# Kernel tuning notes

Hardware: AMD Instinct MI355X
Metric: run time of the kernel (lower is better)

Reference implementation:

```python
import jax, jax.numpy as jnp
import numpy as np

EPS = 0.01    # halting threshold eps
MU = 2.0      # halting probability multiplier
N_MAX = 16    # static upper bound on ACT steps (loop halts in 1-2 steps w/ bias=1, mu=2)

# Binarize: hard threshold at 1-eps forward, straight-through (identity) backward
@jax.custom_vjp
def binarize(x):
    return (x >= 1.0 - EPS).astype(x.dtype)

def _bin_fwd(x):
    return binarize(x), None

def _bin_bwd(_, g):
    return (g,)

binarize.defvjp(_bin_fwd, _bin_bwd)


def setup_inputs() -> dict:
    key = jax.random.key(0)
    ks = jax.random.split(key, 12)
    I, H, O = 4095, 4096, 4096
    sc = 1.0 / np.sqrt(H)
    u = lambda k, s: jax.random.uniform(k, s, jnp.float32, -sc, sc)
    return {
        "x": jax.random.normal(ks[0], (I,), jnp.float32),
        "s0": jax.random.normal(ks[1], (H,), jnp.float32) * 0.1,
        "y0": jax.random.normal(ks[2], (O,), jnp.float32),
        "h0": jnp.zeros((1,), jnp.float32),
        # nn.RNN (tanh) single layer params
        "W_ih": u(ks[3], (H, 1 + I)),
        "b_ih": u(ks[4], (H,)),
        "W_hh": u(ks[5], (H, H)),
        "b_hh": u(ks[6], (H,)),
        # fc_halt (bias hard-set to 1.0 in __init__)
        "W_halt": u(ks[7], (1, H)),
        "b_halt": jnp.ones((1,), jnp.float32),
        # fc_output
        "W_out": u(ks[8], (O, H)),
        "b_out": u(ks[9], (O,)),
    }


def reference(x, s0, y0, h0, W_ih, b_ih, W_hh, b_hh, W_halt, b_halt, W_out, b_out):
    x0 = jnp.concatenate([jnp.zeros((1,), x.dtype), x])  # skip-flag 0 input
    x1 = jnp.concatenate([jnp.ones((1,), x.dtype), x])   # skip-flag 1 input (first step)

    def step(carry, t):
        s, acc = carry
        xin = jnp.where(t == 0, x1, x0)
        valid = acc[0] < 1.0 - EPS  # ACT while-loop condition at step start
        s_new = jnp.tanh(W_ih @ xin + b_ih + W_hh @ s + b_hh)  # tanh RNN cell
        y_new = W_out @ s_new + b_out
        acc_new = acc + MU * jax.nn.sigmoid(W_halt @ s_new + b_halt)
        s_next = jnp.where(valid, s_new, s)
        acc_next = jnp.where(valid, acc_new, acc)
        return (s_next, acc_next), (s_new, y_new, acc_new, valid)

    (_, _), (S, Y, A, V) = jax.lax.scan(step, (s0, h0), jnp.arange(N_MAX))
    # S:[T,H]  Y:[T,O]  A:[T,1]  V:[T] bool
    vmask = V.astype(x.dtype)                 # steps the ACT loop actually executed
    bin_acc = binarize(A[:, 0])               # 0 before halting step, 1 at/after
    halt_bin = bin_acc * vmask                # exactly 1 at the halting step n
    h0_bin = binarize(h0)[0]
    y_sel = jnp.einsum('to,t->o', Y, halt_bin)   # torch.mv(outputs_tensor, bin)
    s_sel = jnp.einsum('th,t->h', S, halt_bin)
    output = h0_bin * y0 + (1.0 - h0_bin) * y_sel
    s = h0_bin * s0 + (1.0 - h0_bin) * s_sel
    ponder = (1.0 - h0_bin) * jnp.sum(vmask * (1.0 - bin_acc))   # = n-1, or 0 if no steps
    last_acc = h0_bin * h0 + (1.0 - h0_bin) * jnp.sum(halt_bin * A[:, 0])[None]
    return (output, s, ponder, last_acc - 1.0)
```

## Files before the change

### kernel.cpp

```cpp
#include <hip/hip_runtime.h>
#include <math.h>


#define H      4096
#define NMAX   16
#define THRESH 0.99f

__device__ __forceinline__ float wave_reduce(float a) {
    #pragma unroll
    for (int off = 32; off > 0; off >>= 1) a += __shfl_down(a, off);
    return a;
}

__global__ __launch_bounds__(256) void k_prep(
    const float* __restrict__ x, float* __restrict__ ws, float* __restrict__ out)
{
    const int i = blockIdx.x * 256 + threadIdx.x;
    if (i < 32) ws[i] = 0.f;
    if (i == 0) out[H] = 0.f;
    if (i < H - 1) out[H + 1 + i] = x[i];
}

__global__ __launch_bounds__(512, 4) void k_step0(
    const float* __restrict__ s0,     const float* __restrict__ h0,
    const float* __restrict__ W_ih,   const float* __restrict__ b_ih,
    const float* __restrict__ W_hh,   const float* __restrict__ b_hh,
    const float* __restrict__ W_halt,
    float* __restrict__ ws, float* __restrict__ out)
{
    if (h0[0] >= THRESH) return;

    const int tid  = threadIdx.x, bid = blockIdx.x;
    const int wave = tid >> 6,   lane = tid & 63;
    const int q    = wave & 3,   m    = wave >> 2;
    const int row  = bid;

    const float4* w4 = (const float4*)((m ? W_hh : W_ih) + (size_t)row * H);
    const float4* v4 = (const float4*)(m ? s0 : (out + H));
    const int base = q * 256 + lane;

    float4 w0 = w4[base      ], w1 = w4[base +  64],
           w2 = w4[base + 128], w3 = w4[base + 192];
    float4 v0 = v4[base      ], v1 = v4[base +  64],
           v2 = v4[base + 128], v3 = v4[base + 192];

    float a0 = w0.x*v0.x + w0.y*v0.y + w0.z*v0.z + w0.w*v0.w
             + w2.x*v2.x + w2.y*v2.y + w2.z*v2.z + w2.w*v2.w;
    float a1 = w1.x*v1.x + w1.y*v1.y + w1.z*v1.z + w1.w*v1.w
             + w3.x*v3.x + w3.y*v3.y + w3.z*v3.z + w3.w*v3.w;
    float a = wave_reduce(a0 + a1);

    __shared__ float part[8];
    if (lane == 0) part[wave] = a;
    __syncthreads();
    if (tid == 0) {
        float z = part[0] + part[1] + part[2] + part[3]
                + part[4] + part[5] + part[6] + part[7]
                + b_ih[row] + b_hh[row] + W_ih[(size_t)row * H];
        float s1 = tanhf(z);
        ws[32 + row] = s1;
        out[row] = W_halt[row] * s1;
    }
}

#define RG   256
#define RT   256

__device__ __forceinline__ void grid_barrier(int* cnt, int* gen) {
    __syncthreads();
    if (threadIdx.x == 0) {
        __threadfence();
        int g = __hip_atomic_load(gen, __ATOMIC_RELAXED, __HIP_MEMORY_SCOPE_AGENT);
        int prev = __hip_atomic_fetch_add(cnt, 1, __ATOMIC_ACQ_REL, __HIP_MEMORY_SCOPE_AGENT);
        if (prev == RG - 1) {
            __hip_atomic_store(cnt, 0, __ATOMIC_RELAXED, __HIP_MEMORY_SCOPE_AGENT);
            __hip_atomic_fetch_add(gen, 1, __ATOMIC_RELEASE, __HIP_MEMORY_SCOPE_AGENT);
        } else {
            while (__hip_atomic_load(gen, __ATOMIC_ACQUIRE, __HIP_MEMORY_SCOPE_AGENT) == g)
                __builtin_amdgcn_s_sleep(8);
        }
        __threadfence();
    }
    __syncthreads();
}

__global__ __launch_bounds__(RT) void k_rest(
    const float* __restrict__ x,
    const float* __restrict__ h0,
    const float* __restrict__ W_ih,   const float* __restrict__ b_ih,
    const float* __restrict__ W_hh,   const float* __restrict__ b_hh,
    const float* __restrict__ W_halt, const float* __restrict__ b_halt,
    const float* __restrict__ hpart,  float* ws)
{
    int* wsI = (int*)ws;
    if (h0[0] >= THRESH) return;

    const int tid = threadIdx.x, bid = blockIdx.x;
    const int wave = tid >> 6, lane = tid & 63;

    {
        const float4* p4 = (const float4*)hpart;
        float a = 0.f;
        #pragma unroll
        for (int j = 0; j < 4; ++j) {
            float4 v = p4[tid + (j << 8)];
            a += v.x + v.y + v.z + v.w;
        }
        a = wave_reduce(a);
        __shared__ float pr[4];
        if (lane == 0) pr[wave] = a;
        __syncthreads();
        float hd  = pr[0] + pr[1] + pr[2] + pr[3];
        float sg  = 1.f / (1.f + expf(-(hd + b_halt[0])));
        float acc0 = h0[0] + 2.f * sg;
        if (acc0 >= THRESH) {
            if (bid == 0 && tid == 0) {
                wsI[4] = 1; wsI[5] = 0; wsI[6] = 0; ws[8] = acc0;
            }
            return;
        }
        if (bid == 0 && tid == 0) { wsI[4] = 0; }
        __syncthreads();
        pr[0] = acc0;
        __syncthreads();
    }

    float* hdot = ws + 16;
    float* sb0  = ws + 32;
    float* sb1  = ws + 32 + H;

    __shared__ float xl[H];
    __shared__ float sl[H];
    if (tid == 0) xl[0] = 0.f;
    for (int i = tid; i < H - 1; i += RT) xl[i + 1] = x[i];

    float acc;
    {
        const float4* p4 = (const float4*)hpart;
        float a = 0.f;
        #pragma unroll
        for (int j = 0; j < 4; ++j) {
            float4 v = p4[tid + (j << 8)];
            a += v.x + v.y + v.z + v.w;
        }
        a = wave_reduce(a);
        __shared__ float pr2[4];
        if (lane == 0) pr2[wave] = a;
        __syncthreads();
        float hd = pr2[0] + pr2[1] + pr2[2] + pr2[3];
        acc = h0[0] + 2.f / (1.f + expf(-(hd + b_halt[0])));
    }
    int   ponder = 1;
    const float bh = b_halt[0];
    bool  halted = false;
    int   sel = 0;
    float last_acc = 0.f;

    for (int t = 1; t < NMAX; ++t) {
        const float* scur = (t & 1) ? sb0 : sb1;
        float*       snew = (t & 1) ? sb1 : sb0;

        __syncthreads();
        for (int i = tid; i < H / 4; i += RT)
            ((float4*)sl)[i] = ((const float4*)scur)[i];
        __syncthreads();

        for (int r = 0; r < 4; ++r) {
            const int row = bid * 16 + r * 4 + wave;
            const float4* wih = (const float4*)(W_ih + (size_t)row * H);
            const float4* whh = (const float4*)(W_hh + (size_t)row * H);
            float a0 = 0.f, a1 = 0.f;
            #pragma unroll 4
            for (int k = 0; k < 16; ++k) {
                const int idx = lane + (k << 6);
                float4 wa = wih[idx], wb = whh[idx];
                float4 va = ((const float4*)xl)[idx], vb = ((const float4*)sl)[idx];
                a0 += wa.x*va.x + wa.y*va.y + wa.z*va.z + wa.w*va.w;
                a1 += wb.x*vb.x + wb.y*vb.y + wb.z*vb.z + wb.w*vb.w;
            }
            float a = wave_reduce(a0 + a1);
            if (lane == 0) {
                float sv = tanhf(a + b_ih[row] + b_hh[row]);
                snew[row] = sv;
                atomicAdd(&hdot[t], W_halt[row] * sv);
            }
        }

        grid_barrier((int*)ws, (int*)ws + 1);

        float hd = ((volatile float*)hdot)[t];
        float sg = 1.f / (1.f + expf(-(hd + bh)));
        acc += 2.f * sg;
        if (acc >= THRESH) { halted = true; last_acc = acc; sel = (t & 1) ? 1 : 0; break; }
        ponder++;
    }

    if (bid == 0 && tid == 0) {
        wsI[4] = halted ? 1 : 0;
        wsI[5] = sel;
        wsI[6] = ponder;
        ws[8]  = last_acc;
    }
}

__global__ __launch_bounds__(512, 4) void k_out(
    const float* __restrict__ s0,    const float* __restrict__ y0,
    const float* __restrict__ h0,
    const float* __restrict__ W_out, const float* __restrict__ b_out,
    const float* __restrict__ ws, float* __restrict__ out)
{
    const float h0v = h0[0];
    const int tid = threadIdx.x, bid = blockIdx.x;

    if (h0v >= THRESH) {
        const int i = bid * 512 + tid;
        if (i < H) { out[i] = y0[i]; out[H + i] = s0[i]; }
        if (i == 0) { out[2*H] = 0.f; out[2*H + 1] = h0v - 1.f; }
        return;
    }

    const int* wsI = (const int*)ws;
    if (!wsI[4]) {
        const int i = bid * 512 + tid;
        if (i < H) { out[i] = 0.f; out[H + i] = 0.f; }
        if (i == 0) { out[2*H] = (float)wsI[6]; out[2*H + 1] = -1.f; }
        return;
    }

    const float* sfin = ws + 32 + (wsI[5] ? H : 0);
    const int wave = tid >> 6, lane = tid & 63;
    const int row  = bid * 2 + (wave >> 2);
    const int q    = wave & 3;

    const float4* w4 = (const float4*)(W_out + (size_t)row * H);
    const float4* v4 = (const float4*)sfin;
    const int base = q * 256 + lane;

    float4 w0 = w4[base      ], w1 = w4[base +  64],
           w2 = w4[base + 128], w3 = w4[base + 192];
    float4 v0 = v4[base      ], v1 = v4[base +  64],
           v2 = v4[base + 128], v3 = v4[base + 192];

    float a0 = w0.x*v0.x + w0.y*v0.y + w0.z*v0.z + w0.w*v0.w
             + w2.x*v2.x + w2.y*v2.y + w2.z*v2.z + w2.w*v2.w;
    float a1 = w1.x*v1.x + w1.y*v1.y + w1.z*v1.z + w1.w*v1.w
             + w3.x*v3.x + w3.y*v3.y + w3.z*v3.z + w3.w*v3.w;
    float a = wave_reduce(a0 + a1);

    __shared__ float part[8];
    if (lane == 0) part[wave] = a;
    __syncthreads();
    if (tid == 0) {
        const int r0 = bid * 2, r1 = r0 + 1;
        out[r0]     = part[0] + part[1] + part[2] + part[3] + b_out[r0];
        out[r1]     = part[4] + part[5] + part[6] + part[7] + b_out[r1];
        out[H + r0] = sfin[r0];
        out[H + r1] = sfin[r1];
        if (bid == 0) {
            out[2*H]     = (float)wsI[6];
            out[2*H + 1] = ws[8] - 1.f;
        }
    }
}

extern "C" void kernel_launch(void* const* d_in, const int* in_sizes, int n_in,
                              void* d_out, int out_size, void* d_ws, size_t ws_size,
                              hipStream_t stream) {
    const float* x      = (const float*)d_in[0];
    const float* s0     = (const float*)d_in[1];
    const float* y0     = (const float*)d_in[2];
    const float* h0     = (const float*)d_in[3];
    const float* W_ih   = (const float*)d_in[4];
    const float* b_ih   = (const float*)d_in[5];
    const float* W_hh   = (const float*)d_in[6];
    const float* b_hh   = (const float*)d_in[7];
    const float* W_halt = (const float*)d_in[8];
    const float* b_halt = (const float*)d_in[9];
    const float* W_out  = (const float*)d_in[10];
    const float* b_out  = (const float*)d_in[11];
    float* out = (float*)d_out;
    float* ws  = (float*)d_ws;

    k_prep<<<dim3(16),   dim3(256), 0, stream>>>(x, ws, out);
    k_step0<<<dim3(4096), dim3(512), 0, stream>>>(
        s0, h0, W_ih, b_ih, W_hh, b_hh, W_halt, ws, out);
    k_rest<<<dim3(RG),   dim3(RT),  0, stream>>>(
        x, h0, W_ih, b_ih, W_hh, b_hh, W_halt, b_halt, out, ws);
    k_out<<<dim3(2048),  dim3(512), 0, stream>>>(
        s0, y0, h0, W_out, b_out, ws, out);
}
```

Baseline: 217.0 us.

## Fuse prep into step0 and use wave-per-row GEMV with LDS vectors

Removes the k_prep kernel and folds workspace zeroing and shifted-x staging into k_step0, which now stages x and s0 in shared memory. Both k_step0 and k_out switch from one row per 512-thread block to one row per wave, eight rows per block. This removes the cross-wave shared-memory reduction and one kernel launch, and cuts the grid from 4096/2048 blocks to 512. It also drops a redundant shared write and barrier in k_rest. The trade-off is that each block now pays an LDS staging cost for the input vectors, and each wave runs a longer serial loop over its row.

```diff
diff --git a/kernel.cpp b/kernel.cpp
--- a/kernel.cpp
+++ b/kernel.cpp
@@ -12,16 +12,8 @@
     return a;
 }
 
-__global__ __launch_bounds__(256) void k_prep(
-    const float* __restrict__ x, float* __restrict__ ws, float* __restrict__ out)
-{
-    const int i = blockIdx.x * 256 + threadIdx.x;
-    if (i < 32) ws[i] = 0.f;
-    if (i == 0) out[H] = 0.f;
-    if (i < H - 1) out[H + 1 + i] = x[i];
-}
-
 __global__ __launch_bounds__(512, 4) void k_step0(
+    const float* __restrict__ x,
     const float* __restrict__ s0,     const float* __restrict__ h0,
     const float* __restrict__ W_ih,   const float* __restrict__ b_ih,
     const float* __restrict__ W_hh,   const float* __restrict__ b_hh,
@@ -32,34 +24,59 @@
 
     const int tid  = threadIdx.x, bid = blockIdx.x;
     const int wave = tid >> 6,   lane = tid & 63;
-    const int q    = wave & 3,   m    = wave >> 2;
-    const int row  = bid;
-
-    const float4* w4 = (const float4*)((m ? W_hh : W_ih) + (size_t)row * H);
-    const float4* v4 = (const float4*)(m ? s0 : (out + H));
-    const int base = q * 256 + lane;
-
-    float4 w0 = w4[base      ], w1 = w4[base +  64],
-           w2 = w4[base + 128], w3 = w4[base + 192];
-    float4 v0 = v4[base      ], v1 = v4[base +  64],
-           v2 = v4[base + 128], v3 = v4[base + 192];
-
-    float a0 = w0.x*v0.x + w0.y*v0.y + w0.z*v0.z + w0.w*v0.w
-             + w2.x*v2.x + w2.y*v2.y + w2.z*v2.z + w2.w*v2.w;
-    float a1 = w1.x*v1.x + w1.y*v1.y + w1.z*v1.z + w1.w*v1.w
-             + w3.x*v3.x + w3.y*v3.y + w3.z*v3.z + w3.w*v3.w;
+
+    if (bid == 0 && tid < 32) ws[tid] = 0.f;
+
+    __shared__ float4 xl[H / 4];
+    __shared__ float4 sl[H / 4];
+
+    {
+        const float4* sg = (const float4*)s0;
+        sl[tid]       = sg[tid];
+        sl[tid + 512] = sg[tid + 512];
+    }
+    {
+        float* xlf = (float*)xl;
+        const float4* x4 = (const float4*)x;
+        for (int j = tid; j < 1023; j += 512) {
+            float4 v = x4[j];
+            const int b = 1 + (j << 2);
+            xlf[b] = v.x; xlf[b + 1] = v.y; xlf[b + 2] = v.z; xlf[b + 3] = v.w;
+        }
+        if (tid == 0) {
+            xlf[0]    = 0.f;
+            xlf[4093] = x[4092];
+            xlf[4094] = x[4093];
+            xlf[4095] = x[4094];
+        }
+    }
+    __syncthreads();
+
+    const int row = (bid << 3) + wave;
+    const float4* wi = (const float4*)(W_ih + (size_t)row * H);
+    const float4* wh = (const float4*)(W_hh + (size_t)row * H);
+
+    const float bi  = b_ih[row];
+    const float bh  = b_hh[row];
+    const float w0c = W_ih[(size_t)row * H];
+    const float whl = W_halt[row];
+
+    float a0 = 0.f, a1 = 0.f;
+    #pragma unroll 8
+    for (int k = 0; k < 16; ++k) {
+        const int idx = lane + (k << 6);
+        float4 wa = wi[idx];
+        float4 wb = wh[idx];
+        float4 va = xl[idx];
+        float4 vb = sl[idx];
+        a0 += wa.x*va.x + wa.y*va.y + wa.z*va.z + wa.w*va.w;
+        a1 += wb.x*vb.x + wb.y*vb.y + wb.z*vb.z + wb.w*vb.w;
+    }
     float a = wave_reduce(a0 + a1);
-
-    __shared__ float part[8];
-    if (lane == 0) part[wave] = a;
-    __syncthreads();
-    if (tid == 0) {
-        float z = part[0] + part[1] + part[2] + part[3]
-                + part[4] + part[5] + part[6] + part[7]
-                + b_ih[row] + b_hh[row] + W_ih[(size_t)row * H];
-        float s1 = tanhf(z);
+    if (lane == 0) {
+        float s1 = tanhf(a + bi + bh + w0c);
         ws[32 + row] = s1;
-        out[row] = W_halt[row] * s1;
+        out[row] = whl * s1;
     }
 }
 
@@ -120,8 +137,6 @@
             return;
         }
         if (bid == 0 && tid == 0) { wsI[4] = 0; }
-        __syncthreads();
-        pr[0] = acc0;
         __syncthreads();
     }
 
@@ -228,38 +243,38 @@
     }
 
     const float* sfin = ws + 32 + (wsI[5] ? H : 0);
+
+    __shared__ float4 vl[H / 4];
+    {
+        const float4* v4 = (const float4*)sfin;
+        vl[tid]       = v4[tid];
+        vl[tid + 512] = v4[tid + 512];
+    }
+    __syncthreads();
+
     const int wave = tid >> 6, lane = tid & 63;
-    const int row  = bid * 2 + (wave >> 2);
-    const int q    = wave & 3;
-
+    const int row  = (bid << 3) + wave;
     const float4* w4 = (const float4*)(W_out + (size_t)row * H);
-    const float4* v4 = (const float4*)sfin;
-    const int base = q * 256 + lane;
-
-    float4 w0 = w4[base      ], w1 = w4[base +  64],
-           w2 = w4[base + 128], w3 = w4[base + 192];
-    float4 v0 = v4[base      ], v1 = v4[base +  64],
-           v2 = v4[base + 128], v3 = v4[base + 192];
-
-    float a0 = w0.x*v0.x + w0.y*v0.y + w0.z*v0.z + w0.w*v0.w
-             + w2.x*v2.x + w2.y*v2.y + w2.z*v2.z + w2.w*v2.w;
-    float a1 = w1.x*v1.x + w1.y*v1.y + w1.z*v1.z + w1.w*v1.w
-             + w3.x*v3.x + w3.y*v3.y + w3.z*v3.z + w3.w*v3.w;
+    const float bo = b_out[row];
+
+    float a0 = 0.f, a1 = 0.f;
+    #pragma unroll 8
+    for (int k = 0; k < 16; k += 2) {
+        const int i0 = lane + (k << 6);
+        const int i1 = lane + ((k + 1) << 6);
+        float4 wa = w4[i0], wb = w4[i1];
+        float4 va = vl[i0], vb = vl[i1];
+        a0 += wa.x*va.x + wa.y*va.y + wa.z*va.z + wa.w*va.w;
+        a1 += wb.x*vb.x + wb.y*vb.y + wb.z*vb.z + wb.w*vb.w;
+    }
     float a = wave_reduce(a0 + a1);
-
-    __shared__ float part[8];
-    if (lane == 0) part[wave] = a;
-    __syncthreads();
-    if (tid == 0) {
-        const int r0 = bid * 2, r1 = r0 + 1;
-        out[r0]     = part[0] + part[1] + part[2] + part[3] + b_out[r0];
-        out[r1]     = part[4] + part[5] + part[6] + part[7] + b_out[r1];
-        out[H + r0] = sfin[r0];
-        out[H + r1] = sfin[r1];
-        if (bid == 0) {
-            out[2*H]     = (float)wsI[6];
-            out[2*H + 1] = ws[8] - 1.f;
-        }
+    if (lane == 0) {
+        out[row]     = a + bo;
+        out[H + row] = ((const float*)vl)[row];
+    }
+    if (bid == 0 && tid == 0) {
+        out[2*H]     = (float)wsI[6];
+        out[2*H + 1] = ws[8] - 1.f;
     }
 }
 
@@ -281,11 +296,10 @@
     float* out = (float*)d_out;
     float* ws  = (float*)d_ws;
 
-    k_prep<<<dim3(16),   dim3(256), 0, stream>>>(x, ws, out);
-    k_step0<<<dim3(4096), dim3(512), 0, stream>>>(
-        s0, h0, W_ih, b_ih, W_hh, b_hh, W_halt, ws, out);
-    k_rest<<<dim3(RG),   dim3(RT),  0, stream>>>(
+    k_step0<<<dim3(512), dim3(512), 0, stream>>>(
+        x, s0, h0, W_ih, b_ih, W_hh, b_hh, W_halt, ws, out);
+    k_rest<<<dim3(RG),  dim3(RT),  0, stream>>>(
         x, h0, W_ih, b_ih, W_hh, b_hh, W_halt, b_halt, out, ws);
-    k_out<<<dim3(2048),  dim3(512), 0, stream>>>(
+    k_out<<<dim3(512),  dim3(512), 0, stream>>>(
         s0, y0, h0, W_out, b_out, ws, out);
 }
```

After: 221.2 us. Within noise of the previous version (+1.9%).
